# Performance work log

Hardware: AMD Instinct MI355X
Metric: run time of the kernel (lower is better)

## Reference

```python
import jax, jax.numpy as jnp
import numpy as np

N = 100000   # num_nodes
R = 8        # num_relations
D = 64       # hidden_dim
E = 3200000  # num_edges


def setup_inputs() -> dict:
    key = jax.random.key(0)
    ks = jax.random.split(key, 10)
    s = 1.0 / np.sqrt(D)
    return {
        "x": jnp.arange(N, dtype=jnp.int64),
        "edge_index": jax.random.randint(ks[0], (2, E), 0, N, dtype=jnp.int64),
        "edge_type": jax.random.randint(ks[1], (E,), 0, R, dtype=jnp.int64),
        "emb": jax.random.normal(ks[2], (N, D), dtype=jnp.float32),
        "W1": jax.random.normal(ks[3], (R, D, D), dtype=jnp.float32) * s,
        "root1": jax.random.normal(ks[4], (D, D), dtype=jnp.float32) * s,
        "b1": jnp.zeros((D,), dtype=jnp.float32),
        "W2": jax.random.normal(ks[5], (R, D, D), dtype=jnp.float32) * s,
        "root2": jax.random.normal(ks[6], (D, D), dtype=jnp.float32) * s,
        "b2": jnp.zeros((D,), dtype=jnp.float32),
    }


def rgcn_conv(h, W, root, b, src, dst, etype):
    # per-edge gather of source features: [E, D]
    msgs = h[src]
    # composite segment id: (dst, relation) -> dst * R + relation
    seg = dst * R + etype
    sums = jax.ops.segment_sum(msgs, seg, num_segments=N * R)          # [N*R, D]
    cnt = jax.ops.segment_sum(jnp.ones((msgs.shape[0],), h.dtype), seg,
                              num_segments=N * R)                       # [N*R]
    mean = sums / jnp.maximum(cnt, 1.0)[:, None]                        # per-relation mean aggr
    mean = mean.reshape(N, R, D)
    # relation-specific transform + root weight + bias
    return jnp.einsum('nrd,rde->ne', mean, W) + h @ root + b


def reference(x, edge_index, edge_type, emb, W1, root1, b1, W2, root2, b2):
    src, dst = edge_index[0], edge_index[1]
    h = emb[x]                                   # embedding lookup
    h = rgcn_conv(h, W1, root1, b1, src, dst, edge_type)
    h = jax.nn.relu(h)                           # dropout = identity (eval mode)
    h = rgcn_conv(h, W2, root2, b2, src, dst, edge_type)
    return h
```

## Files before the change

### kernel.cpp

```cpp
#include <hip/hip_runtime.h>

#define N_NODES 100000
#define R_REL   8
#define D_DIM   64
#define E_EDGES 3200000
#define NSEG    (N_NODES * R_REL)
#define NB      782
#define SEG_PER_BKT 1024
#define BKT_CAP 4800
#define P1_BLOCKS 625
#define P1_CHUNK  5120

typedef __attribute__((ext_vector_type(8))) short short8;
typedef __attribute__((ext_vector_type(4))) float f32x4;

__device__ __forceinline__ unsigned short f2bf(float f) {
    unsigned u = __float_as_uint(f);
    u += 0x7fffu + ((u >> 16) & 1u);
    return (unsigned short)(u >> 16);
}

__device__ __forceinline__ int epack(int s, int d, int r) {
    return (s << 10) | ((d & 127) << 3) | r;
}

__global__ void __launch_bounds__(256)
cvt_kernel(const float* __restrict__ in, unsigned short* __restrict__ outb) {
    size_t base = ((size_t)blockIdx.x * 256 + threadIdx.x) * 8;
    float4 v0 = *(const float4*)(in + base);
    float4 v1 = *(const float4*)(in + base + 4);
    uint4 o;
    o.x = f2bf(v0.x) | ((unsigned)f2bf(v0.y) << 16);
    o.y = f2bf(v0.z) | ((unsigned)f2bf(v0.w) << 16);
    o.z = f2bf(v1.x) | ((unsigned)f2bf(v1.y) << 16);
    o.w = f2bf(v1.z) | ((unsigned)f2bf(v1.w) << 16);
    *(uint4*)(outb + base) = o;
}

__global__ void init_cursor_kernel(int* __restrict__ bkt_cursor) {
    int t = blockIdx.x * 256 + threadIdx.x;
    if (t <= NB) bkt_cursor[t] = t * BKT_CAP;
}

__global__ void __launch_bounds__(256)
p1_scatter_kernel(const int* __restrict__ src, const int* __restrict__ dst,
                  const int* __restrict__ et, int* __restrict__ bkt_cursor,
                  int* __restrict__ packed) {
    __shared__ int hist[NB];
    __shared__ int cur[NB];
    int t = threadIdx.x;
    for (int i = t; i < NB; i += 256) hist[i] = 0;
    __syncthreads();
    int base = blockIdx.x * P1_CHUNK;
    for (int i = t * 4; i < P1_CHUNK; i += 1024) {
        int4 d4 = *(const int4*)(dst + base + i);
        atomicAdd(&hist[d4.x >> 7], 1);
        atomicAdd(&hist[d4.y >> 7], 1);
        atomicAdd(&hist[d4.z >> 7], 1);
        atomicAdd(&hist[d4.w >> 7], 1);
    }
    __syncthreads();
    for (int i = t; i < NB; i += 256) {
        int c = hist[i];
        cur[i] = c ? atomicAdd(&bkt_cursor[i], c) : 0;
    }
    __syncthreads();
    for (int i = t * 4; i < P1_CHUNK; i += 1024) {
        int4 s4 = *(const int4*)(src + base + i);
        int4 d4 = *(const int4*)(dst + base + i);
        int4 t4 = *(const int4*)(et  + base + i);
        int p0 = atomicAdd(&cur[d4.x >> 7], 1); packed[p0] = epack(s4.x, d4.x, t4.x);
        int p1 = atomicAdd(&cur[d4.y >> 7], 1); packed[p1] = epack(s4.y, d4.y, t4.y);
        int p2 = atomicAdd(&cur[d4.z >> 7], 1); packed[p2] = epack(s4.z, d4.z, t4.z);
        int p3 = atomicAdd(&cur[d4.w >> 7], 1); packed[p3] = epack(s4.w, d4.w, t4.w);
    }
}

__global__ void __launch_bounds__(256)
p2_sort_kernel(const int* __restrict__ packed, const int* __restrict__ bkt_cursor,
               int* __restrict__ starts, int* __restrict__ ends, int* __restrict__ esrc) {
    __shared__ int spk[BKT_CAP];
    __shared__ int shist[SEG_PER_BKT];
    __shared__ int scur[SEG_PER_BKT];
    __shared__ int stmp[256];
    int b = blockIdx.x;
    int t = threadIdx.x;
    int ebase = b * BKT_CAP;
    int ecnt  = bkt_cursor[b] - ebase;
    int segbase = b * SEG_PER_BKT;
    int nseg = NSEG - segbase; if (nseg > SEG_PER_BKT) nseg = SEG_PER_BKT;
#pragma unroll
    for (int i = 0; i < 4; ++i) shist[t + i * 256] = 0;
    __syncthreads();
    for (int i = t; i < ecnt; i += 256) {
        int p = packed[ebase + i];
        spk[i] = p;
        atomicAdd(&shist[p & 1023], 1);
    }
    __syncthreads();
    int loc[4], s = 0;
    int b4 = t * 4;
#pragma unroll
    for (int i = 0; i < 4; ++i) { loc[i] = shist[b4 + i]; s += loc[i]; }
    stmp[t] = s;
    __syncthreads();
    for (int off = 1; off < 256; off <<= 1) {
        int x = (t >= off) ? stmp[t - off] : 0;
        __syncthreads();
        stmp[t] += x;
        __syncthreads();
    }
    int run = (t == 0) ? 0 : stmp[t - 1];
#pragma unroll
    for (int i = 0; i < 4; ++i) {
        shist[b4 + i] = run; scur[b4 + i] = run;
        run += loc[i];
    }
    __syncthreads();
    for (int i = t; i < nseg; i += 256)
        starts[segbase + i] = ebase + shist[i];
    for (int i = t; i < ecnt; i += 256) {
        int p = spk[i];
        int r = atomicAdd(&scur[p & 1023], 1);
        esrc[ebase + r] = p >> 10;
    }
    __syncthreads();
    for (int i = t; i < nseg; i += 256)
        ends[segbase + i] = ebase + scur[i];
}

__global__ void wprep_kernel(const float* __restrict__ W, const float* __restrict__ root,
                             unsigned short* __restrict__ wbuf) {
    int r = blockIdx.x;
    const float* src = (r < 8) ? (W + (size_t)r * 4096) : root;
    __shared__ float t[64][65];
    int a = threadIdx.x >> 2, c = threadIdx.x & 3;
#pragma unroll
    for (int i = 0; i < 4; ++i) {
        float4 v = *(const float4*)(src + a * 64 + c * 16 + i * 4);
        t[a][c * 16 + i * 4 + 0] = v.x;
        t[a][c * 16 + i * 4 + 1] = v.y;
        t[a][c * 16 + i * 4 + 2] = v.z;
        t[a][c * 16 + i * 4 + 3] = v.w;
    }
    __syncthreads();
    unsigned short* outrow = wbuf + (size_t)r * 4096 + a * 64;
#pragma unroll
    for (int i = 0; i < 4; ++i) {
        int k0 = c * 16 + i * 4;
        ushort4 o;
        o.x = f2bf(t[k0 + 0][a]); o.y = f2bf(t[k0 + 1][a]);
        o.z = f2bf(t[k0 + 2][a]); o.w = f2bf(t[k0 + 3][a]);
        *(ushort4*)(outrow + k0) = o;
    }
}

__global__ void __launch_bounds__(512, 6)
fused_kernel(const unsigned short* __restrict__ hb, const int* __restrict__ esrc,
             const int* __restrict__ starts, const int* __restrict__ ends,
             const unsigned short* __restrict__ wbuf, const float* __restrict__ bias,
             void* __restrict__ out, int mode) {
    __shared__ unsigned short As[8][32][72];
    int tid = threadIdx.x;
    int g   = tid >> 4;
    int ml  = tid & 15;
    int n0  = blockIdx.x * 32;

    {
        int segb = (n0 + g) * R_REL;
        int4 eA = *(const int4*)(ends + segb);
        int4 eB = *(const int4*)(ends + segb + 4);
        int beg_cur = starts[segb];
        int end_cur = eA.x;
        int eN = eB.w;
        int r = 0;
        float a0 = 0.f, a1 = 0.f, a2 = 0.f, a3 = 0.f;

#define FLUSH()                                                          \
    do {                                                                 \
        float inv = __builtin_amdgcn_rcpf(                               \
            fmaxf((float)(end_cur - beg_cur), 1.0f));                    \
        ushort4 o;                                                       \
        o.x = f2bf(a0 * inv); o.y = f2bf(a1 * inv);                      \
        o.z = f2bf(a2 * inv); o.w = f2bf(a3 * inv);                      \
        *(ushort4*)(&As[r][g][ml * 4]) = o;                              \
        a0 = a1 = a2 = a3 = 0.f;                                         \
        ++r;                                                             \
        beg_cur = end_cur;                                               \
        end_cur = (r == 1) ? eA.y : (r == 2) ? eA.z : (r == 3) ? eA.w :  \
                  (r == 4) ? eB.x : (r == 5) ? eB.y : (r == 6) ? eB.z :  \
                  (r == 7) ? eB.w : 0x7fffffff;                          \
    } while (0)

#define LOAD8(IDS, ROWS, EB)                                             \
    do {                                                                 \
        _Pragma("unroll")                                                \
        for (int i = 0; i < 8; ++i) {                                    \
            int ee = (EB) + i; ee = (ee < eN) ? ee : (eN - 1);           \
            IDS[i] = esrc[ee];                                           \
        }                                                                \
        _Pragma("unroll")                                                \
        for (int i = 0; i < 8; ++i)                                      \
            ROWS[i] = *(const uint2*)(hb + (size_t)IDS[i] * D_DIM + ml * 4); \
    } while (0)

#define ACC8(ROWS, EB)                                                   \
    do {                                                                 \
        _Pragma("unroll")                                                \
        for (int i = 0; i < 8; ++i) {                                    \
            while ((EB) + i >= end_cur) FLUSH();                         \
            float msk = ((EB) + i < eN) ? 1.0f : 0.0f;                   \
            a0 = fmaf(msk, __uint_as_float(ROWS[i].x << 16), a0);        \
            a1 = fmaf(msk, __uint_as_float(ROWS[i].x & 0xffff0000u), a1);\
            a2 = fmaf(msk, __uint_as_float(ROWS[i].y << 16), a2);        \
            a3 = fmaf(msk, __uint_as_float(ROWS[i].y & 0xffff0000u), a3);\
        }                                                                \
    } while (0)

        int idsA[8], idsB[8];
        uint2 rowsA[8], rowsB[8];
        if (beg_cur < eN) {
            int e = beg_cur;
            LOAD8(idsA, rowsA, e);
            while (true) {
                LOAD8(idsB, rowsB, e + 8);
                ACC8(rowsA, e);
                e += 8;
                if (e >= eN) break;
                LOAD8(idsA, rowsA, e + 8);
                ACC8(rowsB, e);
                e += 8;
                if (e >= eN) break;
            }
        }
        while (r < 8) FLUSH();
#undef FLUSH
#undef LOAD8
#undef ACC8
    }

    int w  = tid >> 6;
    int kg = g & 3;
    int h  = w & 1;
    int q  = w >> 1;

    const unsigned short* rp = hb + (size_t)(n0 + h * 16 + ml) * D_DIM + kg * 8;
    short8 RA0 = *(const short8*)(rp);
    short8 RA1 = *(const short8*)(rp + 32);

    __syncthreads();

    f32x4 acc = {0, 0, 0, 0};
#pragma unroll 1
    for (int p = 0; p < 8; ++p) {
        short8 A0 = *(const short8*)(&As[p][h * 16 + ml][kg * 8]);
        short8 A1 = *(const short8*)(&As[p][h * 16 + ml][kg * 8 + 32]);
        const unsigned short* bp = wbuf + (size_t)p * 4096 + (q * 16 + ml) * 64 + kg * 8;
        short8 B0 = *(const short8*)(bp);
        short8 B1 = *(const short8*)(bp + 32);
        acc = __builtin_amdgcn_mfma_f32_16x16x32_bf16(A0, B0, acc, 0, 0, 0);
        acc = __builtin_amdgcn_mfma_f32_16x16x32_bf16(A1, B1, acc, 0, 0, 0);
    }
    {
        const unsigned short* bp = wbuf + (size_t)8 * 4096 + (q * 16 + ml) * 64 + kg * 8;
        short8 B0 = *(const short8*)(bp);
        short8 B1 = *(const short8*)(bp + 32);
        acc = __builtin_amdgcn_mfma_f32_16x16x32_bf16(RA0, B0, acc, 0, 0, 0);
        acc = __builtin_amdgcn_mfma_f32_16x16x32_bf16(RA1, B1, acc, 0, 0, 0);
    }

    float bv = bias[q * 16 + ml];
#pragma unroll
    for (int rg = 0; rg < 4; ++rg) {
        int node = n0 + h * 16 + kg * 4 + rg;
        float v = acc[rg] + bv;
        if (mode) {
            v = fmaxf(v, 0.f);
            ((unsigned short*)out)[(size_t)node * D_DIM + q * 16 + ml] = f2bf(v);
        } else {
            ((float*)out)[(size_t)node * D_DIM + q * 16 + ml] = v;
        }
    }
}


extern "C" void kernel_launch(void* const* d_in, const int* in_sizes, int n_in,
                              void* d_out, int out_size, void* d_ws, size_t ws_size,
                              hipStream_t stream) {
    const int*   ei    = (const int*)d_in[1];
    const int*   src   = ei;
    const int*   dst   = ei + E_EDGES;
    const int*   et    = (const int*)d_in[2];
    const float* emb   = (const float*)d_in[3];
    const float* W1    = (const float*)d_in[4];
    const float* root1 = (const float*)d_in[5];
    const float* b1    = (const float*)d_in[6];
    const float* W2    = (const float*)d_in[7];
    const float* root2 = (const float*)d_in[8];
    const float* b2    = (const float*)d_in[9];
    float*       out   = (float*)d_out;

    unsigned short* embb   = (unsigned short*)d_ws;
    unsigned short* h1b    = embb + (size_t)N_NODES * D_DIM;
    unsigned short* wbuf1  = h1b + (size_t)N_NODES * D_DIM;
    unsigned short* wbuf2  = wbuf1 + 9 * 4096;
    int*            starts = (int*)(wbuf2 + 9 * 4096);
    int*            ends   = starts + NSEG;
    int*            packed = ends + NSEG;
    int*            esrc   = packed + (size_t)NB * BKT_CAP;
    int*            bkt_cursor = esrc + (size_t)NB * BKT_CAP;

    init_cursor_kernel<<<4, 256, 0, stream>>>(bkt_cursor);
    p1_scatter_kernel <<<P1_BLOCKS, 256, 0, stream>>>(src, dst, et, bkt_cursor, packed);
    p2_sort_kernel    <<<NB, 256, 0, stream>>>(packed, bkt_cursor, starts, ends, esrc);

    wprep_kernel<<<9, 256, 0, stream>>>(W1, root1, wbuf1);
    wprep_kernel<<<9, 256, 0, stream>>>(W2, root2, wbuf2);
    cvt_kernel<<<(N_NODES * D_DIM) / 2048, 256, 0, stream>>>(emb, embb);

    const int blocks = N_NODES / 32;

    fused_kernel<<<blocks, 512, 0, stream>>>(embb, esrc, starts, ends, wbuf1, b1, h1b, 1);
    fused_kernel<<<blocks, 512, 0, stream>>>(h1b, esrc, starts, ends, wbuf2, b2, out, 0);
}
```

Baseline: 444.5 us.

## Distribute segment-pair aggregation via shared-memory work pool instead of one node per group

Replaces the fixed one-node-per-16-thread-group gather loop with a dynamic work queue. Groups atomically claim pairs of (node, relation) segments from a shared counter, and segment start/end offsets are staged in shared memory first. The aim is to balance the uneven edge counts across groups within a block and keep two independent gather streams in flight per group. In exchange it adds LDS atomics, shuffles and branchy partial loads of four rows at a time instead of the previous eight-deep software pipeline.

```diff
diff --git a/kernel.cpp b/kernel.cpp
--- a/kernel.cpp
+++ b/kernel.cpp
@@ -161,86 +161,79 @@
              const unsigned short* __restrict__ wbuf, const float* __restrict__ bias,
              void* __restrict__ out, int mode) {
     __shared__ unsigned short As[8][32][72];
+    __shared__ int sS[256], sE[256];
+    __shared__ int pool;
     int tid = threadIdx.x;
-    int g   = tid >> 4;
     int ml  = tid & 15;
     int n0  = blockIdx.x * 32;
-
-    {
-        int segb = (n0 + g) * R_REL;
-        int4 eA = *(const int4*)(ends + segb);
-        int4 eB = *(const int4*)(ends + segb + 4);
-        int beg_cur = starts[segb];
-        int end_cur = eA.x;
-        int eN = eB.w;
-        int r = 0;
-        float a0 = 0.f, a1 = 0.f, a2 = 0.f, a3 = 0.f;
-
-#define FLUSH()                                                          \
-    do {                                                                 \
-        float inv = __builtin_amdgcn_rcpf(                               \
-            fmaxf((float)(end_cur - beg_cur), 1.0f));                    \
-        ushort4 o;                                                       \
-        o.x = f2bf(a0 * inv); o.y = f2bf(a1 * inv);                      \
-        o.z = f2bf(a2 * inv); o.w = f2bf(a3 * inv);                      \
-        *(ushort4*)(&As[r][g][ml * 4]) = o;                              \
-        a0 = a1 = a2 = a3 = 0.f;                                         \
-        ++r;                                                             \
-        beg_cur = end_cur;                                               \
-        end_cur = (r == 1) ? eA.y : (r == 2) ? eA.z : (r == 3) ? eA.w :  \
-                  (r == 4) ? eB.x : (r == 5) ? eB.y : (r == 6) ? eB.z :  \
-                  (r == 7) ? eB.w : 0x7fffffff;                          \
-    } while (0)
-
-#define LOAD8(IDS, ROWS, EB)                                             \
+    int sblk = n0 * R_REL;
+
+    if (tid < 256) sS[tid] = starts[sblk + tid];
+    else           sE[tid - 256] = ends[sblk + tid - 256];
+    if (tid == 0) pool = 0;
+    __syncthreads();
+
+#define ACC4(P0,P1,P2,P3, RW, M)                                         \
     do {                                                                 \
         _Pragma("unroll")                                                \
-        for (int i = 0; i < 8; ++i) {                                    \
-            int ee = (EB) + i; ee = (ee < eN) ? ee : (eN - 1);           \
-            IDS[i] = esrc[ee];                                           \
+        for (int i = 0; i < 4; ++i) if (i < (M)) {                       \
+            P0 += __uint_as_float(RW[i].x << 16);                        \
+            P1 += __uint_as_float(RW[i].x & 0xffff0000u);                \
+            P2 += __uint_as_float(RW[i].y << 16);                        \
+            P3 += __uint_as_float(RW[i].y & 0xffff0000u);                \
         }                                                                \
-        _Pragma("unroll")                                                \
-        for (int i = 0; i < 8; ++i)                                      \
-            ROWS[i] = *(const uint2*)(hb + (size_t)IDS[i] * D_DIM + ml * 4); \
     } while (0)
 
-#define ACC8(ROWS, EB)                                                   \
+#define LOAD4(RW, B, E)                                                  \
     do {                                                                 \
         _Pragma("unroll")                                                \
-        for (int i = 0; i < 8; ++i) {                                    \
-            while ((EB) + i >= end_cur) FLUSH();                         \
-            float msk = ((EB) + i < eN) ? 1.0f : 0.0f;                   \
-            a0 = fmaf(msk, __uint_as_float(ROWS[i].x << 16), a0);        \
-            a1 = fmaf(msk, __uint_as_float(ROWS[i].x & 0xffff0000u), a1);\
-            a2 = fmaf(msk, __uint_as_float(ROWS[i].y << 16), a2);        \
-            a3 = fmaf(msk, __uint_as_float(ROWS[i].y & 0xffff0000u), a3);\
+        for (int i = 0; i < 4; ++i) {                                    \
+            int ee = (B) + i; ee = (ee < (E)) ? ee : ((E) - 1);          \
+            int sid = esrc[ee];                                          \
+            RW[i] = *(const uint2*)(hb + (size_t)sid * D_DIM + ml * 4);  \
         }                                                                \
     } while (0)
 
-        int idsA[8], idsB[8];
-        uint2 rowsA[8], rowsB[8];
-        if (beg_cur < eN) {
-            int e = beg_cur;
-            LOAD8(idsA, rowsA, e);
-            while (true) {
-                LOAD8(idsB, rowsB, e + 8);
-                ACC8(rowsA, e);
-                e += 8;
-                if (e >= eN) break;
-                LOAD8(idsA, rowsA, e + 8);
-                ACC8(rowsB, e);
-                e += 8;
-                if (e >= eN) break;
-            }
+    while (true) {
+        int s2 = 0;
+        if (ml == 0) s2 = atomicAdd(&pool, 2);
+        s2 = __shfl(s2, 0, 16);
+        if (s2 >= 256) break;
+        int b0 = sS[s2],     e0 = sE[s2];
+        int b1 = sS[s2 + 1], e1 = sE[s2 + 1];
+        int c0 = e0 - b0, c1 = e1 - b1;
+        float p0 = 0.f, p1 = 0.f, p2 = 0.f, p3 = 0.f;
+        float q0 = 0.f, q1 = 0.f, q2 = 0.f, q3 = 0.f;
+        while (b0 < e0 || b1 < e1) {
+            int m0 = e0 - b0; m0 = (m0 > 4) ? 4 : m0;
+            int m1 = e1 - b1; m1 = (m1 > 4) ? 4 : m1;
+            uint2 rA[4], rB[4];
+            if (m0 > 0) LOAD4(rA, b0, e0);
+            if (m1 > 0) LOAD4(rB, b1, e1);
+            if (m0 > 0) { ACC4(p0, p1, p2, p3, rA, m0); b0 += m0; }
+            if (m1 > 0) { ACC4(q0, q1, q2, q3, rB, m1); b1 += m1; }
         }
-        while (r < 8) FLUSH();
-#undef FLUSH
-#undef LOAD8
-#undef ACC8
-    }
+        int nl = s2 >> 3, r = s2 & 7;
+        {
+            float inv = __builtin_amdgcn_rcpf(fmaxf((float)c0, 1.0f));
+            ushort4 o;
+            o.x = f2bf(p0 * inv); o.y = f2bf(p1 * inv);
+            o.z = f2bf(p2 * inv); o.w = f2bf(p3 * inv);
+            *(ushort4*)(&As[r][nl][ml * 4]) = o;
+        }
+        {
+            float inv = __builtin_amdgcn_rcpf(fmaxf((float)c1, 1.0f));
+            ushort4 o;
+            o.x = f2bf(q0 * inv); o.y = f2bf(q1 * inv);
+            o.z = f2bf(q2 * inv); o.w = f2bf(q3 * inv);
+            *(ushort4*)(&As[r + 1][nl][ml * 4]) = o;
+        }
+    }
+#undef ACC4
+#undef LOAD4
 
     int w  = tid >> 6;
-    int kg = g & 3;
+    int kg = (tid >> 4) & 3;
     int h  = w & 1;
     int q  = w >> 1;
 
```

Result: slower. 459.8 us (+3.4%).

## Stage block edge-source indices in LDS, merge prep kernels, simplify gather loop

Applied to the files above, without the earlier changes.

The fused kernel now copies each block's contiguous range of edge-source indices into shared memory before aggregating, so the per-edge index loads come from LDS rather than global memory. The gather loop loses its double-buffered A/B prefetch and becomes a single 8-wide batch per iteration, with accumulation done as packed float2 adds under an edge-count guard. The two weight-prep launches and the embedding conversion launch are merged into one prep kernel to cut launch overhead. The LDS buffer is a fixed 1536 ints, so a block whose 32 nodes have more incoming edges than that would overflow it. Dropping the prefetch also reduces memory-level parallelism in the gather.

```diff
diff --git a/kernel.cpp b/kernel.cpp
--- a/kernel.cpp
+++ b/kernel.cpp
@@ -10,9 +10,11 @@
 #define BKT_CAP 4800
 #define P1_BLOCKS 625
 #define P1_CHUNK  5120
+#define ESRC_CAP 1536
 
 typedef __attribute__((ext_vector_type(8))) short short8;
 typedef __attribute__((ext_vector_type(4))) float f32x4;
+typedef __attribute__((ext_vector_type(2))) float f32x2;
 
 __device__ __forceinline__ unsigned short f2bf(float f) {
     unsigned u = __float_as_uint(f);
@@ -22,19 +24,6 @@
 
 __device__ __forceinline__ int epack(int s, int d, int r) {
     return (s << 10) | ((d & 127) << 3) | r;
-}
-
-__global__ void __launch_bounds__(256)
-cvt_kernel(const float* __restrict__ in, unsigned short* __restrict__ outb) {
-    size_t base = ((size_t)blockIdx.x * 256 + threadIdx.x) * 8;
-    float4 v0 = *(const float4*)(in + base);
-    float4 v1 = *(const float4*)(in + base + 4);
-    uint4 o;
-    o.x = f2bf(v0.x) | ((unsigned)f2bf(v0.y) << 16);
-    o.y = f2bf(v0.z) | ((unsigned)f2bf(v0.w) << 16);
-    o.z = f2bf(v1.x) | ((unsigned)f2bf(v1.y) << 16);
-    o.w = f2bf(v1.z) | ((unsigned)f2bf(v1.w) << 16);
-    *(uint4*)(outb + base) = o;
 }
 
 __global__ void init_cursor_kernel(int* __restrict__ bkt_cursor) {
@@ -129,29 +118,49 @@
         ends[segbase + i] = ebase + scur[i];
 }
 
-__global__ void wprep_kernel(const float* __restrict__ W, const float* __restrict__ root,
-                             unsigned short* __restrict__ wbuf) {
-    int r = blockIdx.x;
-    const float* src = (r < 8) ? (W + (size_t)r * 4096) : root;
-    __shared__ float t[64][65];
-    int a = threadIdx.x >> 2, c = threadIdx.x & 3;
-#pragma unroll
-    for (int i = 0; i < 4; ++i) {
-        float4 v = *(const float4*)(src + a * 64 + c * 16 + i * 4);
-        t[a][c * 16 + i * 4 + 0] = v.x;
-        t[a][c * 16 + i * 4 + 1] = v.y;
-        t[a][c * 16 + i * 4 + 2] = v.z;
-        t[a][c * 16 + i * 4 + 3] = v.w;
-    }
-    __syncthreads();
-    unsigned short* outrow = wbuf + (size_t)r * 4096 + a * 64;
-#pragma unroll
-    for (int i = 0; i < 4; ++i) {
-        int k0 = c * 16 + i * 4;
-        ushort4 o;
-        o.x = f2bf(t[k0 + 0][a]); o.y = f2bf(t[k0 + 1][a]);
-        o.z = f2bf(t[k0 + 2][a]); o.w = f2bf(t[k0 + 3][a]);
-        *(ushort4*)(outrow + k0) = o;
+__global__ void __launch_bounds__(256)
+prep_kernel(const float* __restrict__ W1, const float* __restrict__ root1,
+            const float* __restrict__ W2, const float* __restrict__ root2,
+            const float* __restrict__ emb,
+            unsigned short* __restrict__ wbuf1, unsigned short* __restrict__ wbuf2,
+            unsigned short* __restrict__ embb) {
+    int b = blockIdx.x;
+    if (b < 18) {
+        int r = (b < 9) ? b : b - 9;
+        const float* W    = (b < 9) ? W1 : W2;
+        const float* root = (b < 9) ? root1 : root2;
+        unsigned short* wbuf = (b < 9) ? wbuf1 : wbuf2;
+        const float* src = (r < 8) ? (W + (size_t)r * 4096) : root;
+        __shared__ float t[64][65];
+        int a = threadIdx.x >> 2, c = threadIdx.x & 3;
+#pragma unroll
+        for (int i = 0; i < 4; ++i) {
+            float4 v = *(const float4*)(src + a * 64 + c * 16 + i * 4);
+            t[a][c * 16 + i * 4 + 0] = v.x;
+            t[a][c * 16 + i * 4 + 1] = v.y;
+            t[a][c * 16 + i * 4 + 2] = v.z;
+            t[a][c * 16 + i * 4 + 3] = v.w;
+        }
+        __syncthreads();
+        unsigned short* outrow = wbuf + (size_t)r * 4096 + a * 64;
+#pragma unroll
+        for (int i = 0; i < 4; ++i) {
+            int k0 = c * 16 + i * 4;
+            ushort4 o;
+            o.x = f2bf(t[k0 + 0][a]); o.y = f2bf(t[k0 + 1][a]);
+            o.z = f2bf(t[k0 + 2][a]); o.w = f2bf(t[k0 + 3][a]);
+            *(ushort4*)(outrow + k0) = o;
+        }
+    } else {
+        size_t base = ((size_t)(b - 18) * 256 + threadIdx.x) * 8;
+        float4 v0 = *(const float4*)(emb + base);
+        float4 v1 = *(const float4*)(emb + base + 4);
+        uint4 o;
+        o.x = f2bf(v0.x) | ((unsigned)f2bf(v0.y) << 16);
+        o.y = f2bf(v0.z) | ((unsigned)f2bf(v0.w) << 16);
+        o.z = f2bf(v1.x) | ((unsigned)f2bf(v1.y) << 16);
+        o.w = f2bf(v1.z) | ((unsigned)f2bf(v1.w) << 16);
+        *(uint4*)(embb + base) = o;
     }
 }
 
@@ -161,30 +170,39 @@
              const unsigned short* __restrict__ wbuf, const float* __restrict__ bias,
              void* __restrict__ out, int mode) {
     __shared__ unsigned short As[8][32][72];
+    __shared__ int esrc_lds[ESRC_CAP];
     int tid = threadIdx.x;
     int g   = tid >> 4;
     int ml  = tid & 15;
     int n0  = blockIdx.x * 32;
+    int sblk = n0 * R_REL;
+
+    int E0 = starts[sblk];
+    int L  = ends[sblk + 255] - E0;
+    for (int i = tid; i < L; i += 512) esrc_lds[i] = esrc[E0 + i];
+    __syncthreads();
 
     {
-        int segb = (n0 + g) * R_REL;
+        int segb = sblk + g * R_REL;
         int4 eA = *(const int4*)(ends + segb);
         int4 eB = *(const int4*)(ends + segb + 4);
-        int beg_cur = starts[segb];
+        int beg_cur = starts[segb] - E0;
+        eA.x -= E0; eA.y -= E0; eA.z -= E0; eA.w -= E0;
+        eB.x -= E0; eB.y -= E0; eB.z -= E0; eB.w -= E0;
         int end_cur = eA.x;
         int eN = eB.w;
         int r = 0;
-        float a0 = 0.f, a1 = 0.f, a2 = 0.f, a3 = 0.f;
+        f32x2 a01 = {0.f, 0.f}, a23 = {0.f, 0.f};
 
 #define FLUSH()                                                          \
     do {                                                                 \
         float inv = __builtin_amdgcn_rcpf(                               \
             fmaxf((float)(end_cur - beg_cur), 1.0f));                    \
         ushort4 o;                                                       \
-        o.x = f2bf(a0 * inv); o.y = f2bf(a1 * inv);                      \
-        o.z = f2bf(a2 * inv); o.w = f2bf(a3 * inv);                      \
+        o.x = f2bf(a01.x * inv); o.y = f2bf(a01.y * inv);                \
+        o.z = f2bf(a23.x * inv); o.w = f2bf(a23.y * inv);                \
         *(ushort4*)(&As[r][g][ml * 4]) = o;                              \
-        a0 = a1 = a2 = a3 = 0.f;                                         \
+        a01 = (f32x2){0.f, 0.f}; a23 = (f32x2){0.f, 0.f};                \
         ++r;                                                             \
         beg_cur = end_cur;                                               \
         end_cur = (r == 1) ? eA.y : (r == 2) ? eA.z : (r == 3) ? eA.w :  \
@@ -192,51 +210,33 @@
                   (r == 7) ? eB.w : 0x7fffffff;                          \
     } while (0)
 
-#define LOAD8(IDS, ROWS, EB)                                             \
-    do {                                                                 \
-        _Pragma("unroll")                                                \
-        for (int i = 0; i < 8; ++i) {                                    \
-            int ee = (EB) + i; ee = (ee < eN) ? ee : (eN - 1);           \
-            IDS[i] = esrc[ee];                                           \
-        }                                                                \
-        _Pragma("unroll")                                                \
-        for (int i = 0; i < 8; ++i)                                      \
-            ROWS[i] = *(const uint2*)(hb + (size_t)IDS[i] * D_DIM + ml * 4); \
-    } while (0)
-
-#define ACC8(ROWS, EB)                                                   \
-    do {                                                                 \
-        _Pragma("unroll")                                                \
-        for (int i = 0; i < 8; ++i) {                                    \
-            while ((EB) + i >= end_cur) FLUSH();                         \
-            float msk = ((EB) + i < eN) ? 1.0f : 0.0f;                   \
-            a0 = fmaf(msk, __uint_as_float(ROWS[i].x << 16), a0);        \
-            a1 = fmaf(msk, __uint_as_float(ROWS[i].x & 0xffff0000u), a1);\
-            a2 = fmaf(msk, __uint_as_float(ROWS[i].y << 16), a2);        \
-            a3 = fmaf(msk, __uint_as_float(ROWS[i].y & 0xffff0000u), a3);\
-        }                                                                \
-    } while (0)
-
-        int idsA[8], idsB[8];
-        uint2 rowsA[8], rowsB[8];
-        if (beg_cur < eN) {
-            int e = beg_cur;
-            LOAD8(idsA, rowsA, e);
-            while (true) {
-                LOAD8(idsB, rowsB, e + 8);
-                ACC8(rowsA, e);
-                e += 8;
-                if (e >= eN) break;
-                LOAD8(idsA, rowsA, e + 8);
-                ACC8(rowsB, e);
-                e += 8;
-                if (e >= eN) break;
+        int e = beg_cur;
+        while (e < eN) {
+            int m = eN - e; if (m > 8) m = 8;
+            uint2 rows[8];
+#pragma unroll
+            for (int i = 0; i < 8; ++i) {
+                int ee = e + i; ee = (ee < eN) ? ee : (eN - 1);
+                int sid = esrc_lds[ee];
+                rows[i] = *(const uint2*)(hb + (size_t)sid * D_DIM + ml * 4);
             }
+#pragma unroll
+            for (int i = 0; i < 8; ++i) {
+                if (i < m) {
+                    while (e + i >= end_cur) FLUSH();
+                    f32x2 u, v;
+                    u.x = __uint_as_float(rows[i].x << 16);
+                    u.y = __uint_as_float(rows[i].x & 0xffff0000u);
+                    v.x = __uint_as_float(rows[i].y << 16);
+                    v.y = __uint_as_float(rows[i].y & 0xffff0000u);
+                    a01 += u;
+                    a23 += v;
+                }
+            }
+            e += m;
         }
         while (r < 8) FLUSH();
 #undef FLUSH
-#undef LOAD8
-#undef ACC8
     }
 
     int w  = tid >> 6;
@@ -314,9 +314,8 @@
     p1_scatter_kernel <<<P1_BLOCKS, 256, 0, stream>>>(src, dst, et, bkt_cursor, packed);
     p2_sort_kernel    <<<NB, 256, 0, stream>>>(packed, bkt_cursor, starts, ends, esrc);
 
-    wprep_kernel<<<9, 256, 0, stream>>>(W1, root1, wbuf1);
-    wprep_kernel<<<9, 256, 0, stream>>>(W2, root2, wbuf2);
-    cvt_kernel<<<(N_NODES * D_DIM) / 2048, 256, 0, stream>>>(emb, embb);
+    prep_kernel<<<18 + (N_NODES * D_DIM) / 2048, 256, 0, stream>>>(
+        W1, root1, W2, root2, emb, wbuf1, wbuf2, embb);
 
     const int blocks = N_NODES / 32;
 
```

After: 418.5 us. 1.06x faster.
